# Kernel optimization log

Measured on AMD Instinct MI355X. Metric: run time of the kernel, lower is better.

The kernel has to match this reference:

```python
import jax, jax.numpy as jnp
import numpy as np

D_MODEL = 1024
NUM_HEAD = 16
D_HEAD = D_MODEL // NUM_HEAD


def setup_inputs() -> dict:
    key = jax.random.key(0)
    kx, kq, kk, kv, ko = jax.random.split(key, 5)
    x = jax.random.normal(kx, (2, 2048, D_MODEL), dtype=jnp.float32)
    p_q = jax.random.normal(kq, (D_MODEL, D_MODEL), dtype=jnp.float32)
    p_k = jax.random.normal(kk, (D_MODEL, D_MODEL), dtype=jnp.float32)
    p_v = jax.random.normal(kv, (D_MODEL, D_MODEL), dtype=jnp.float32)
    p_o = jax.random.normal(ko, (D_MODEL, D_MODEL), dtype=jnp.float32)
    return {"x": x, "p_q": p_q, "p_k": p_k, "p_v": p_v, "p_o": p_o}


def reference(x, p_q, p_k, p_v, p_o):
    B, S, _ = x.shape
    # project: weight viewed as [H, d_head, d_model]; out[b,h,s,d] = sum_m x[b,s,m] W[h,d,m]
    wq = p_q.reshape(NUM_HEAD, D_HEAD, D_MODEL)
    wk = p_k.reshape(NUM_HEAD, D_HEAD, D_MODEL)
    wv = p_v.reshape(NUM_HEAD, D_HEAD, D_MODEL)
    q = jnp.einsum('bsm,hdm->bhsd', x, wq)
    k = jnp.einsum('bsm,hdm->bhsd', x, wk)
    v = jnp.einsum('bsm,hdm->bhsd', x, wv)
    # full causal attention, scores scaled by 1/sqrt(d_head)
    scores = jnp.einsum('bhqd,bhkd->bhqk', q, k) / jnp.sqrt(jnp.float32(D_HEAD))
    causal = jnp.tril(jnp.ones((S, S), dtype=bool))
    scores = jnp.where(causal, scores, -jnp.inf)
    attn = jax.nn.softmax(scores, axis=-1)
    out = jnp.einsum('bhqk,bhkd->bhqd', attn, v)
    out = out.transpose(0, 2, 1, 3).reshape(B, S, D_MODEL)  # [B,S,H*d_head]
    # output proj: einsum '... d1, d2 d1 -> ... d2' == out @ p_o.T
    return jnp.einsum('bsm,nm->bsn', out, p_o)
```

## Files before the change

### kernel.cpp

```cpp
#include <hip/hip_runtime.h>
#include <stdint.h>

#define D_MODEL 1024
#define SEQ     2048
#define NHEAD   16
#define BATCH   2
#define NROWS   (BATCH*SEQ)

typedef _Float16 f16;
typedef _Float16 f16x8 __attribute__((ext_vector_type(8)));
typedef _Float16 f16x4 __attribute__((ext_vector_type(4)));
typedef __fp16   h16x2 __attribute__((ext_vector_type(2)));
typedef float    f32x4 __attribute__((ext_vector_type(4)));

#define MFMA16 __builtin_amdgcn_mfma_f32_16x16x32_f16

__device__ __forceinline__ void gload16(const void* g, void* l) {
  __builtin_amdgcn_global_load_lds(
      (const __attribute__((address_space(1))) void*)g,
      (__attribute__((address_space(3))) void*)l, 16, 0, 0);
}

__device__ __forceinline__ int pkh2(float a, float b) {
  union { h16x2 h; int i; } u;
  u.h = __builtin_amdgcn_cvt_pkrtz(a, b);
  return u.i;
}

__global__ void split4_kernel(const float* __restrict__ in, f16* __restrict__ hi,
                              f16* __restrict__ lo, int n4, float scale) {
  int i = blockIdx.x * blockDim.x + threadIdx.x;
  if (i >= n4) return;
  float4 v = reinterpret_cast<const float4*>(in)[i];
  v.x *= scale; v.y *= scale; v.z *= scale; v.w *= scale;
  f16x4 h, l4;
  h[0] = (f16)v.x; h[1] = (f16)v.y; h[2] = (f16)v.z; h[3] = (f16)v.w;
  l4[0] = (f16)(v.x - (float)h[0]);
  l4[1] = (f16)(v.y - (float)h[1]);
  l4[2] = (f16)(v.z - (float)h[2]);
  l4[3] = (f16)(v.w - (float)h[3]);
  *reinterpret_cast<f16x4*>(hi + 4*(size_t)i) = h;
  *reinterpret_cast<f16x4*>(lo + 4*(size_t)i) = l4;
}

__global__ void prep_w_kernel(const float* __restrict__ pq, const float* __restrict__ pk,
                              const float* __restrict__ pv, const float* __restrict__ po,
                              f16* __restrict__ wq_hi, f16* __restrict__ wq_lo,
                              f16* __restrict__ wk_hi, f16* __restrict__ wk_lo,
                              f16* __restrict__ wv_h,  f16* __restrict__ wo_h,
                              int n4, float qscale) {
  int i = blockIdx.x * blockDim.x + threadIdx.x;
  if (i >= n4) return;
  {
    float4 v = reinterpret_cast<const float4*>(pq)[i];
    v.x *= qscale; v.y *= qscale; v.z *= qscale; v.w *= qscale;
    f16x4 h, l4;
    h[0] = (f16)v.x; h[1] = (f16)v.y; h[2] = (f16)v.z; h[3] = (f16)v.w;
    l4[0] = (f16)(v.x - (float)h[0]); l4[1] = (f16)(v.y - (float)h[1]);
    l4[2] = (f16)(v.z - (float)h[2]); l4[3] = (f16)(v.w - (float)h[3]);
    *reinterpret_cast<f16x4*>(wq_hi + 4*(size_t)i) = h;
    *reinterpret_cast<f16x4*>(wq_lo + 4*(size_t)i) = l4;
  }
  {
    float4 v = reinterpret_cast<const float4*>(pk)[i];
    f16x4 h, l4;
    h[0] = (f16)v.x; h[1] = (f16)v.y; h[2] = (f16)v.z; h[3] = (f16)v.w;
    l4[0] = (f16)(v.x - (float)h[0]); l4[1] = (f16)(v.y - (float)h[1]);
    l4[2] = (f16)(v.z - (float)h[2]); l4[3] = (f16)(v.w - (float)h[3]);
    *reinterpret_cast<f16x4*>(wk_hi + 4*(size_t)i) = h;
    *reinterpret_cast<f16x4*>(wk_lo + 4*(size_t)i) = l4;
  }
  {
    float4 v = reinterpret_cast<const float4*>(pv)[i];
    f16x4 h;
    h[0] = (f16)v.x; h[1] = (f16)v.y; h[2] = (f16)v.z; h[3] = (f16)v.w;
    *reinterpret_cast<f16x4*>(wv_h + 4*(size_t)i) = h;
  }
  {
    float4 v = reinterpret_cast<const float4*>(po)[i];
    f16x4 h;
    h[0] = (f16)v.x; h[1] = (f16)v.y; h[2] = (f16)v.z; h[3] = (f16)v.w;
    *reinterpret_cast<f16x4*>(wo_h + 4*(size_t)i) = h;
  }
}

template<bool F32_OUT, bool COLCHUNK>
__global__ __launch_bounds__(256, 2)
void gemm_nt(const f16* __restrict__ Ahi,
             const f16* __restrict__ Bhi,
             f16* __restrict__ Chi, float* __restrict__ Cf,
             int M, int N, int K)
{
  constexpr int B_OFF  = 8192;
  constexpr int STRIDE = 12288;
  __shared__ __align__(16) char smem[2 * STRIDE];

  const int tid = threadIdx.x;
  const int w = tid >> 6, l = tid & 63;
  const int wr = (w >> 1) * 64;
  const int wc = (w & 1) * 32;

  const int gx = gridDim.x, gy = gridDim.y;
  const int nwg = gx * gy;
  const int flat = blockIdx.y * gx + blockIdx.x;
  const int swz = (flat & 7) * (nwg >> 3) + (flat >> 3);
  const int bxn = COLCHUNK ? (swz / gy) : (swz % gx);
  const int byn = COLCHUNK ? (swz % gy) : (swz / gx);
  const int bm = byn * 128, bn = bxn * 64;

  f32x4 acc[4][2] = {};

  const int srow = tid >> 2;
  const int schunk = 8 * (((tid & 3) ^ ((srow >> 1) & 3)));

  auto stage = [&](int kt) {
    char* dst = smem + (kt & 1) * STRIDE;
    const int k0 = kt * 32;
    const f16* ga = Ahi + (size_t)(bm + srow) * K + k0 + schunk;
    gload16(ga,        dst + (w << 10));
    gload16(ga + 64*K, dst + 4096 + (w << 10));
    const f16* gb = Bhi + (size_t)(bn + srow) * K + k0 + schunk;
    gload16(gb,        dst + B_OFF + (w << 10));
  };

  const int nkt = K >> 5;
  stage(0);

  for (int kt = 0; kt < nkt; kt++) {
    if (kt + 1 < nkt) {
      stage(kt + 1);
      asm volatile("s_waitcnt vmcnt(3)" ::: "memory");
    } else {
      asm volatile("s_waitcnt vmcnt(0)" ::: "memory");
    }
    __builtin_amdgcn_s_barrier();

    const char* buf = smem + (kt & 1) * STRIDE;
    const int ar = (l & 15);
    const int ak = 16 * ((l >> 4) ^ ((ar >> 1) & 3));
    f16x8 a_hi[4];
#pragma unroll
    for (int mi = 0; mi < 4; mi++)
      a_hi[mi] = *(const f16x8*)(buf + (size_t)(wr + mi*16 + ar) * 64 + ak);
    __builtin_amdgcn_s_setprio(1);
#pragma unroll
    for (int ni = 0; ni < 2; ni++) {
      f16x8 b_hi = *(const f16x8*)(buf + B_OFF + (size_t)(wc + ni*16 + ar) * 64 + ak);
#pragma unroll
      for (int mi = 0; mi < 4; mi++)
        acc[mi][ni] = MFMA16(a_hi[mi], b_hi, acc[mi][ni], 0, 0, 0);
    }
    __builtin_amdgcn_s_setprio(0);
    __builtin_amdgcn_s_barrier();
  }

  const int crow0 = bm + wr + (l >> 4) * 4;
  const int ccol0 = bn + wc + (l & 15);
#pragma unroll
  for (int mi = 0; mi < 4; mi++) {
#pragma unroll
    for (int ni = 0; ni < 2; ni++) {
#pragma unroll
      for (int j = 0; j < 4; j++) {
        size_t idx = (size_t)(crow0 + mi*16 + j) * N + (ccol0 + ni*16);
        float v = acc[mi][ni][j];
        if (F32_OUT) Cf[idx] = v;
        else         Chi[idx] = (f16)v;
      }
    }
  }
}

__global__ __launch_bounds__(256, 2)
void gemm_qkv(const f16* __restrict__ Ahi, const f16* __restrict__ Alo,
              const f16* __restrict__ Bqh, const f16* __restrict__ Bql,
              const f16* __restrict__ Bkh, const f16* __restrict__ Bkl,
              const f16* __restrict__ Bvh,
              f16* __restrict__ Qh, f16* __restrict__ Qlo2,
              f16* __restrict__ Kh, f16* __restrict__ Klo2,
              f16* __restrict__ VT)
{
  constexpr int N = D_MODEL, K = D_MODEL;
  constexpr int STRIDE = 36864;
  __shared__ __align__(16) char smem[2 * STRIDE];

  const int tid = threadIdx.x;
  const int w = tid >> 6, l = tid & 63;
  const int wr = (w >> 1) * 64;
  const int wc = (w & 1) * 32;

  const int flat = blockIdx.y * 16 + blockIdx.x;
  const int swz = (flat & 7) * 64 + (flat >> 3);
  const int bm = (swz / 16) * 128, bn = (swz % 16) * 64;

  f32x4 accQ[4][2] = {}, accK[4][2] = {}, accV[4][2] = {};

  const int srow = tid >> 2;
  const int schunk = 8 * (((tid & 3) ^ ((srow >> 1) & 3)));

  auto stage = [&](int kt) {
    char* dst = smem + (kt & 1) * STRIDE;
    const int k0 = kt * 32;
    const f16* ga = Ahi + (size_t)(bm + srow) * K + k0 + schunk;
    gload16(ga,        dst + (w << 10));
    gload16(ga + 64*K, dst + 4096 + (w << 10));
    const f16* gal = Alo + (size_t)(bm + srow) * K + k0 + schunk;
    gload16(gal,        dst + 8192 + (w << 10));
    gload16(gal + 64*K, dst + 12288 + (w << 10));
    const size_t bo = (size_t)(bn + srow) * K + k0 + schunk;
    gload16(Bqh + bo, dst + 16384 + (w << 10));
    gload16(Bql + bo, dst + 20480 + (w << 10));
    gload16(Bkh + bo, dst + 24576 + (w << 10));
    gload16(Bkl + bo, dst + 28672 + (w << 10));
    gload16(Bvh + bo, dst + 32768 + (w << 10));
  };

  const int nkt = K >> 5;
  stage(0);

  for (int kt = 0; kt < nkt; kt++) {
    if (kt + 1 < nkt) {
      stage(kt + 1);
      asm volatile("s_waitcnt vmcnt(9)" ::: "memory");
    } else {
      asm volatile("s_waitcnt vmcnt(0)" ::: "memory");
    }
    __builtin_amdgcn_s_barrier();

    const char* buf = smem + (kt & 1) * STRIDE;
    const int ar = (l & 15);
    const int ak = 16 * ((l >> 4) ^ ((ar >> 1) & 3));
    f16x8 a_hi[4], a_lo[4];
#pragma unroll
    for (int mi = 0; mi < 4; mi++) {
      a_hi[mi] = *(const f16x8*)(buf + (size_t)(wr + mi*16 + ar) * 64 + ak);
      a_lo[mi] = *(const f16x8*)(buf + 8192 + (size_t)(wr + mi*16 + ar) * 64 + ak);
    }
    __builtin_amdgcn_s_setprio(1);
#pragma unroll
    for (int ni = 0; ni < 2; ni++) {
      const int bo = (wc + ni*16 + ar) * 64 + ak;
      f16x8 bqh = *(const f16x8*)(buf + 16384 + bo);
      f16x8 bql = *(const f16x8*)(buf + 20480 + bo);
      f16x8 bkh = *(const f16x8*)(buf + 24576 + bo);
      f16x8 bkl = *(const f16x8*)(buf + 28672 + bo);
      f16x8 bvh = *(const f16x8*)(buf + 32768 + bo);
#pragma unroll
      for (int mi = 0; mi < 4; mi++) {
        accQ[mi][ni] = MFMA16(a_hi[mi], bqh, accQ[mi][ni], 0, 0, 0);
        accQ[mi][ni] = MFMA16(a_hi[mi], bql, accQ[mi][ni], 0, 0, 0);
        accQ[mi][ni] = MFMA16(a_lo[mi], bqh, accQ[mi][ni], 0, 0, 0);
        accK[mi][ni] = MFMA16(a_hi[mi], bkh, accK[mi][ni], 0, 0, 0);
        accK[mi][ni] = MFMA16(a_hi[mi], bkl, accK[mi][ni], 0, 0, 0);
        accK[mi][ni] = MFMA16(a_lo[mi], bkh, accK[mi][ni], 0, 0, 0);
        accV[mi][ni] = MFMA16(a_hi[mi], bvh, accV[mi][ni], 0, 0, 0);
      }
    }
    __builtin_amdgcn_s_setprio(0);
    __builtin_amdgcn_s_barrier();
  }

  const int crow0 = bm + wr + (l >> 4) * 4;
  const int ccol0 = bn + wc + (l & 15);
#pragma unroll
  for (int mi = 0; mi < 4; mi++) {
#pragma unroll
    for (int ni = 0; ni < 2; ni++) {
#pragma unroll
      for (int j = 0; j < 4; j++) {
        size_t idx = (size_t)(crow0 + mi*16 + j) * N + (ccol0 + ni*16);
        float qv = accQ[mi][ni][j];
        f16 qh = (f16)qv;
        Qh[idx] = qh;  Qlo2[idx] = (f16)(qv - (float)qh);
        float kv = accK[mi][ni][j];
        f16 kh = (f16)kv;
        Kh[idx] = kh;  Klo2[idx] = (f16)(kv - (float)kh);
      }
    }
  }

  {
    f16* tl = (f16*)smem;
#pragma unroll
    for (int mi = 0; mi < 4; mi++) {
#pragma unroll
      for (int ni = 0; ni < 2; ni++) {
        f16x4 v;
#pragma unroll
        for (int j = 0; j < 4; j++) v[j] = (f16)accV[mi][ni][j];
        const int m_l = wc + ni*16 + (l & 15);
        const int n_l = wr + mi*16 + ((l >> 4) << 2);
        *reinterpret_cast<f16x4*>(tl + m_l*136 + n_l) = v;
      }
    }
    __syncthreads();
    const int m_l = tid >> 2, cg = tid & 3;
    const size_t vbase = (size_t)(bn + m_l) * NROWS + bm + cg*32;
#pragma unroll
    for (int k2 = 0; k2 < 4; k2++) {
      f16x8 v = *reinterpret_cast<const f16x8*>(tl + m_l*136 + cg*32 + k2*8);
      *reinterpret_cast<f16x8*>(VT + vbase + k2*8) = v;
    }
  }
}

__global__ __launch_bounds__(512, 4)
void attn_kernel(const f16* __restrict__ Qhi, const f16* __restrict__ Qlo,
                 const f16* __restrict__ Khi, const f16* __restrict__ Klo,
                 const f16* __restrict__ VT, f16* __restrict__ Out)
{
  __shared__ __align__(16) char smem[49152];

  const int tid = threadIdx.x, w = tid >> 6, l = tid & 63;
  const int g = l >> 4, q4 = l & 15;
  const int wi = w & 3, grp = w >> 2;
  const int flat = blockIdx.x;
  const int xcd = flat & 7, slot = flat >> 3;
  const int bh = xcd * 4 + (slot >> 4);
  const int c = slot & 15;
  const int b = bh >> 4, h = bh & 15;
  const int bS = b * SEQ;
  const size_t hoff = (size_t)h * 64;
  const int T  = 64 - 2 * c;
  const int P1 = 2 * c + 2;
  const int P2 = 31 - 2 * c;

  int qw = (grp ? (31 - c) : c) * 64 + wi * 16;

  f16x8 qh[2], ql[2];
  auto loadQ = [&]() {
#pragma unroll
    for (int ks = 0; ks < 2; ks++) {
      const size_t base = (size_t)(bS + qw + q4) * D_MODEL + hoff + ks * 32 + g * 8;
      qh[ks] = *(const f16x8*)(Qhi + base);
      ql[ks] = *(const f16x8*)(Qlo + base);
    }
  };
  loadQ();

  f32x4 o[4] = {};
  float m_run = -INFINITY, l_run = 0.f;

  const int k_src = 8 * ((l & 7) ^ (l >> 3));
  const int v_src = 8 * ((l & 3) ^ ((l >> 2) & 3));
  const int rowloc = w * 8 + (l >> 3);

  const int idx_lo = (q4 + 32 * (g & 1)) * 4;
  const int idx_hi = idx_lo + 64;
  const bool upper = (l >= 32);

  auto stage64 = [&](int t) {
    const int kv0 = t * 64;
    char* dst = smem + (t & 1) * 24576;
    const size_t krow = (size_t)(bS + kv0 + rowloc) * D_MODEL + hoff + k_src;
    gload16(Khi + krow, dst + (w << 10));
    gload16(Klo + krow, dst + 8192 + (w << 10));
    const size_t vrow = (hoff + rowloc) * (size_t)NROWS + bS + kv0 + k_src;
    gload16(VT + vrow, dst + 16384 + (w << 10));
  };

  auto compute64 = [&](int t) {
    const char* buf = smem + (t & 1) * 24576;
    const int kv0 = t * 64;

    f32x4 s[4] = {};
    __builtin_amdgcn_s_setprio(1);
#pragma unroll
    for (int ni = 0; ni < 4; ni++) {
      const int row = ni * 16 + q4;
#pragma unroll
      for (int ks = 0; ks < 2; ks++) {
        const int boff = row * 128 + 16 * ((ks * 4 + g) ^ (row & 7));
        f16x8 kh8 = *(const f16x8*)(buf + boff);
        f16x8 kl8 = *(const f16x8*)(buf + 8192 + boff);
        s[ni] = MFMA16(kh8, qh[ks], s[ni], 0, 0, 0);
        s[ni] = MFMA16(kh8, ql[ks], s[ni], 0, 0, 0);
        s[ni] = MFMA16(kl8, qh[ks], s[ni], 0, 0, 0);
      }
    }
    __builtin_amdgcn_s_setprio(0);

    const bool need_mask = (kv0 + 63) > qw;
    const int q_abs = qw + q4;
    float p[4][4];
    float pm = -INFINITY;
#pragma unroll
    for (int ni = 0; ni < 4; ni++)
#pragma unroll
      for (int j = 0; j < 4; j++) {
        float v = s[ni][j];
        if (need_mask && (kv0 + ni * 16 + 4 * g + j) > q_abs) v = -INFINITY;
        p[ni][j] = v;
        pm = fmaxf(pm, v);
      }
    pm = fmaxf(pm, __shfl_xor(pm, 16));
    pm = fmaxf(pm, __shfl_xor(pm, 32));

    if (!__all(pm - m_run <= 8.0f)) {
      const float mn = fmaxf(m_run, pm);
      const float sc2 = __builtin_amdgcn_exp2f(m_run - mn);
      m_run = mn;
      l_run *= sc2;
#pragma unroll
      for (int nd = 0; nd < 4; nd++)
#pragma unroll
        for (int j = 0; j < 4; j++) o[nd][j] *= sc2;
    }
    float ps = 0.f;
#pragma unroll
    for (int ni = 0; ni < 4; ni++)
#pragma unroll
      for (int j = 0; j < 4; j++) {
        const float e = __builtin_amdgcn_exp2f(p[ni][j] - m_run);
        p[ni][j] = e;
        ps += e;
      }
    ps += __shfl_xor(ps, 16);
    ps += __shfl_xor(ps, 32);
    l_run += ps;

    f16x8 pa[2];
#pragma unroll
    for (int h2 = 0; h2 < 2; h2++) {
      const int pk0 = pkh2(p[2*h2][0],   p[2*h2][1]);
      const int pk1 = pkh2(p[2*h2][2],   p[2*h2][3]);
      const int pk2 = pkh2(p[2*h2+1][0], p[2*h2+1][1]);
      const int pk3 = pkh2(p[2*h2+1][2], p[2*h2+1][3]);
      const int b0l = __builtin_amdgcn_ds_bpermute(idx_lo, pk0);
      const int b2l = __builtin_amdgcn_ds_bpermute(idx_lo, pk2);
      const int b1l = __builtin_amdgcn_ds_bpermute(idx_lo, pk1);
      const int b3l = __builtin_amdgcn_ds_bpermute(idx_lo, pk3);
      const int b0h = __builtin_amdgcn_ds_bpermute(idx_hi, pk0);
      const int b2h = __builtin_amdgcn_ds_bpermute(idx_hi, pk2);
      const int b1h = __builtin_amdgcn_ds_bpermute(idx_hi, pk1);
      const int b3h = __builtin_amdgcn_ds_bpermute(idx_hi, pk3);
      union { int u[4]; f16x8 v; } pu;
      pu.u[0] = upper ? b2l : b0l;
      pu.u[1] = upper ? b3l : b1l;
      pu.u[2] = upper ? b2h : b0h;
      pu.u[3] = upper ? b3h : b1h;
      pa[h2] = pu.v;
    }

    __builtin_amdgcn_s_setprio(1);
#pragma unroll
    for (int nd = 0; nd < 4; nd++) {
      const int d = nd * 16 + q4;
#pragma unroll
      for (int h2 = 0; h2 < 2; h2++) {
        f16x8 bv = *(const f16x8*)(buf + 16384 + d * 128 + 16 * ((h2 * 4 + g) ^ (d & 7)));
        o[nd] = MFMA16(bv, pa[h2], o[nd], 0, 0, 0);
      }
    }
    __builtin_amdgcn_s_setprio(0);
  };

  auto stage32 = [&](int t) {
    const int kv0 = t * 32;
    char* sb = smem + (t & 3) * 12288;
    if (w < 4) {
      const f16* src = (w < 2) ? Khi : Klo;
      char* dstc = sb + ((w < 2) ? 0 : 4096);
      const int wi2 = w & 1;
#pragma unroll
      for (int gi = 0; gi < 2; gi++) {
        const int sub = 2 * wi2 + gi;
        const int row = 8 * sub + (l >> 3);
        gload16(src + (size_t)(bS + kv0 + row) * D_MODEL + hoff + k_src,
                dstc + sub * 1024);
      }
    } else if (w < 6) {
      const int wi2 = w - 4;
#pragma unroll
      for (int gi = 0; gi < 2; gi++) {
        const int sub = 2 * wi2 + gi;
        const int drow = 16 * sub + (l >> 2);
        gload16(VT + (hoff + drow) * (size_t)NROWS + bS + kv0 + v_src,
                sb + 8192 + sub * 1024);
      }
    }
  };

  auto compute32 = [&](int t) {
    const char* sb = smem + (t & 3) * 12288;
    const int kv0 = t * 32;

    f32x4 s[2] = {};
    __builtin_amdgcn_s_setprio(1);
#pragma unroll
    for (int ni = 0; ni < 2; ni++) {
      const int row = ni * 16 + q4;
#pragma unroll
      for (int ks = 0; ks < 2; ks++) {
        const int boff = row * 128 + 16 * ((ks * 4 + g) ^ (row & 7));
        f16x8 kh8 = *(const f16x8*)(sb + boff);
        f16x8 kl8 = *(const f16x8*)(sb + 4096 + boff);
        s[ni] = MFMA16(kh8, qh[ks], s[ni], 0, 0, 0);
        s[ni] = MFMA16(kh8, ql[ks], s[ni], 0, 0, 0);
        s[ni] = MFMA16(kl8, qh[ks], s[ni], 0, 0, 0);
      }
    }
    __builtin_amdgcn_s_setprio(0);

    const bool need_mask = (kv0 + 31) > qw;
    const int q_abs = qw + q4;
    float p[2][4];
    float pm = -INFINITY;
#pragma unroll
    for (int ni = 0; ni < 2; ni++)
#pragma unroll
      for (int j = 0; j < 4; j++) {
        float v = s[ni][j];
        if (need_mask && (kv0 + ni * 16 + 4 * g + j) > q_abs) v = -INFINITY;
        p[ni][j] = v;
        pm = fmaxf(pm, v);
      }
    pm = fmaxf(pm, __shfl_xor(pm, 16));
    pm = fmaxf(pm, __shfl_xor(pm, 32));

    if (!__all(pm - m_run <= 8.0f)) {
      const float mn = fmaxf(m_run, pm);
      const float sc2 = __builtin_amdgcn_exp2f(m_run - mn);
      m_run = mn;
      l_run *= sc2;
#pragma unroll
      for (int nd = 0; nd < 4; nd++)
#pragma unroll
        for (int j = 0; j < 4; j++) o[nd][j] *= sc2;
    }
    float ps = 0.f;
#pragma unroll
    for (int ni = 0; ni < 2; ni++)
#pragma unroll
      for (int j = 0; j < 4; j++) {
        const float e = __builtin_amdgcn_exp2f(p[ni][j] - m_run);
        p[ni][j] = e;
        ps += e;
      }
    ps += __shfl_xor(ps, 16);
    ps += __shfl_xor(ps, 32);
    l_run += ps;

    const int pk0 = pkh2(p[0][0], p[0][1]);
    const int pk1 = pkh2(p[0][2], p[0][3]);
    const int pk2 = pkh2(p[1][0], p[1][1]);
    const int pk3 = pkh2(p[1][2], p[1][3]);
    const int b0l = __builtin_amdgcn_ds_bpermute(idx_lo, pk0);
    const int b2l = __builtin_amdgcn_ds_bpermute(idx_lo, pk2);
    const int b1l = __builtin_amdgcn_ds_bpermute(idx_lo, pk1);
    const int b3l = __builtin_amdgcn_ds_bpermute(idx_lo, pk3);
    const int b0h = __builtin_amdgcn_ds_bpermute(idx_hi, pk0);
    const int b2h = __builtin_amdgcn_ds_bpermute(idx_hi, pk2);
    const int b1h = __builtin_amdgcn_ds_bpermute(idx_hi, pk1);
    const int b3h = __builtin_amdgcn_ds_bpermute(idx_hi, pk3);
    union { int u[4]; f16x8 v; } pu;
    pu.u[0] = upper ? b2l : b0l;
    pu.u[1] = upper ? b3l : b1l;
    pu.u[2] = upper ? b2h : b0h;
    pu.u[3] = upper ? b3h : b1h;
    const f16x8 pa = pu.v;

    __builtin_amdgcn_s_setprio(1);
#pragma unroll
    for (int nd = 0; nd < 4; nd++) {
      const int d = nd * 16 + q4;
      f16x8 bv = *(const f16x8*)(sb + 8192 + d * 64 + 16 * (g ^ (d & 3)));
      o[nd] = MFMA16(bv, pa, o[nd], 0, 0, 0);
    }
    __builtin_amdgcn_s_setprio(0);
  };

  stage64(0);
  for (int t = 0; t <= c; t++) {
    if (t + 1 <= c) {
      stage64(t + 1);
      asm volatile("s_waitcnt vmcnt(3)" ::: "memory");
    } else {
      asm volatile("s_waitcnt vmcnt(0)" ::: "memory");
    }
    __builtin_amdgcn_s_barrier();
    compute64(t);
    __builtin_amdgcn_s_barrier();
  }

  if (grp == 0) {
    const float inv = 1.0f / l_run;
    const size_t rowb = (size_t)(bS + qw + q4) * D_MODEL + hoff;
#pragma unroll
    for (int nd = 0; nd < 4; nd++) {
      f16x4 v;
#pragma unroll
      for (int j = 0; j < 4; j++) v[j] = (f16)(o[nd][j] * inv);
      *reinterpret_cast<f16x4*>(Out + rowb + nd * 16 + 4 * g) = v;
    }
    qw = (31 - c) * 64 + wi * 16;
    loadQ();
#pragma unroll
    for (int nd = 0; nd < 4; nd++)
#pragma unroll
      for (int j = 0; j < 4; j++) o[nd][j] = 0.f;
    m_run = -INFINITY;
    l_run = 0.f;
  }

  stage32(P1);
  stage32(P1 + 1);
  for (int j = 0; j < P2; j++) {
    const int u = P1 + 2 * j;
    const bool st = (u + 3) < T;
    if (st) { stage32(u + 2); stage32(u + 3); }
    if (st) asm volatile("s_waitcnt vmcnt(4)" ::: "memory");
    else    asm volatile("s_waitcnt vmcnt(0)" ::: "memory");
    __builtin_amdgcn_s_barrier();
    compute32(u + grp);
    __builtin_amdgcn_s_barrier();
  }

  if (grp == 0) {
    float* mb = (float*)smem + wi * 1152 + l * 18;
#pragma unroll
    for (int nd = 0; nd < 4; nd++)
#pragma unroll
      for (int j = 0; j < 4; j++) mb[nd * 4 + j] = o[nd][j];
    mb[16] = m_run;
    mb[17] = l_run;
  }
  __syncthreads();
  if (grp == 1) {
    const float* mb = (const float*)smem + wi * 1152 + l * 18;
    const float m2 = mb[16], l2 = mb[17];
    const float mm = fmaxf(m_run, m2);
    const float a1 = __builtin_amdgcn_exp2f(m_run - mm);
    const float a2 = __builtin_amdgcn_exp2f(m2 - mm);
    const float inv = 1.0f / (l_run * a1 + l2 * a2);
    const size_t rowb = (size_t)(bS + qw + q4) * D_MODEL + hoff;
#pragma unroll
    for (int nd = 0; nd < 4; nd++) {
      f16x4 v;
#pragma unroll
      for (int j = 0; j < 4; j++)
        v[j] = (f16)((o[nd][j] * a1 + mb[nd * 4 + j] * a2) * inv);
      *reinterpret_cast<f16x4*>(Out + rowb + nd * 16 + 4 * g) = v;
    }
  }
}

extern "C" void kernel_launch(void* const* d_in, const int* in_sizes, int n_in,
                              void* d_out, int out_size, void* d_ws, size_t ws_size,
                              hipStream_t stream) {
  const float* x  = (const float*)d_in[0];
  const float* pq = (const float*)d_in[1];
  const float* pk = (const float*)d_in[2];
  const float* pv = (const float*)d_in[3];
  const float* po = (const float*)d_in[4];
  float* out = (float*)d_out;

  char* ws = (char*)d_ws;
  size_t off = 0;
  auto alloc = [&](size_t elems) {
    f16* p = (f16*)(ws + off);
    off += ((elems * 2 + 255) & ~(size_t)255);
    return p;
  };
  f16* x_hi  = alloc((size_t)NROWS * D_MODEL);
  f16* x_lo  = alloc((size_t)NROWS * D_MODEL);
  f16* wq_hi = alloc((size_t)D_MODEL * D_MODEL);
  f16* wq_lo = alloc((size_t)D_MODEL * D_MODEL);
  f16* wk_hi = alloc((size_t)D_MODEL * D_MODEL);
  f16* wk_lo = alloc((size_t)D_MODEL * D_MODEL);
  f16* wv_h  = alloc((size_t)D_MODEL * D_MODEL);
  f16* wo_h  = alloc((size_t)D_MODEL * D_MODEL);
  f16* q_hi  = alloc((size_t)NROWS * D_MODEL);
  f16* q_lo  = alloc((size_t)NROWS * D_MODEL);
  f16* k_hi  = alloc((size_t)NROWS * D_MODEL);
  f16* k_lo  = alloc((size_t)NROWS * D_MODEL);
  f16* vt    = alloc((size_t)NROWS * D_MODEL);
  f16* ao    = alloc((size_t)NROWS * D_MODEL);

  const int n4x = NROWS * D_MODEL / 4;
  const int n4w = D_MODEL * D_MODEL / 4;
  const float qscale = 0.125f * 1.44269504088896f;
  split4_kernel<<<n4x/256, 256, 0, stream>>>(x, x_hi, x_lo, n4x, 1.0f);
  prep_w_kernel<<<n4w/256, 256, 0, stream>>>(pq, pk, pv, po,
                                             wq_hi, wq_lo, wk_hi, wk_lo, wv_h, wo_h,
                                             n4w, qscale);

  gemm_qkv<<<dim3(16, 32), 256, 0, stream>>>(x_hi, x_lo, wq_hi, wq_lo, wk_hi, wk_lo,
                                             wv_h, q_hi, q_lo, k_hi, k_lo, vt);

  attn_kernel<<<dim3(512), 512, 0, stream>>>(q_hi, q_lo, k_hi, k_lo, vt, ao);

  dim3 gg(D_MODEL/64, NROWS/128);
  gemm_nt<true, false><<<gg, 256, 0, stream>>>(ao, wo_h, nullptr, out, NROWS, D_MODEL, D_MODEL);
}
```

Measured before the change: 157.0 us.

## Replace 32-wide second-phase KV tiles with 64-wide triple-buffered tiles

```diff
diff --git a/kernel.cpp b/kernel.cpp
--- a/kernel.cpp
+++ b/kernel.cpp
@@ -309,7 +309,7 @@
                  const f16* __restrict__ Khi, const f16* __restrict__ Klo,
                  const f16* __restrict__ VT, f16* __restrict__ Out)
 {
-  __shared__ __align__(16) char smem[49152];
+  __shared__ __align__(16) char smem[73728];
 
   const int tid = threadIdx.x, w = tid >> 6, l = tid & 63;
   const int g = l >> 4, q4 = l & 15;
@@ -321,9 +321,7 @@
   const int b = bh >> 4, h = bh & 15;
   const int bS = b * SEQ;
   const size_t hoff = (size_t)h * 64;
-  const int T  = 64 - 2 * c;
-  const int P1 = 2 * c + 2;
-  const int P2 = 31 - 2 * c;
+  const int TB = 31 - c;
 
   int qw = (grp ? (31 - c) : c) * 64 + wi * 16;
 
@@ -342,16 +340,15 @@
   float m_run = -INFINITY, l_run = 0.f;
 
   const int k_src = 8 * ((l & 7) ^ (l >> 3));
-  const int v_src = 8 * ((l & 3) ^ ((l >> 2) & 3));
   const int rowloc = w * 8 + (l >> 3);
 
   const int idx_lo = (q4 + 32 * (g & 1)) * 4;
   const int idx_hi = idx_lo + 64;
   const bool upper = (l >= 32);
 
-  auto stage64 = [&](int t) {
+  auto stage64 = [&](int t, int slot3) {
     const int kv0 = t * 64;
-    char* dst = smem + (t & 1) * 24576;
+    char* dst = smem + slot3 * 24576;
     const size_t krow = (size_t)(bS + kv0 + rowloc) * D_MODEL + hoff + k_src;
     gload16(Khi + krow, dst + (w << 10));
     gload16(Klo + krow, dst + 8192 + (w << 10));
@@ -359,8 +356,8 @@
     gload16(VT + vrow, dst + 16384 + (w << 10));
   };
 
-  auto compute64 = [&](int t) {
-    const char* buf = smem + (t & 1) * 24576;
+  auto compute64 = [&](int t, int slot3) {
+    const char* buf = smem + slot3 * 24576;
     const int kv0 = t * 64;
 
     f32x4 s[4] = {};
@@ -455,131 +452,16 @@
     __builtin_amdgcn_s_setprio(0);
   };
 
-  auto stage32 = [&](int t) {
-    const int kv0 = t * 32;
-    char* sb = smem + (t & 3) * 12288;
-    if (w < 4) {
-      const f16* src = (w < 2) ? Khi : Klo;
-      char* dstc = sb + ((w < 2) ? 0 : 4096);
-      const int wi2 = w & 1;
-#pragma unroll
-      for (int gi = 0; gi < 2; gi++) {
-        const int sub = 2 * wi2 + gi;
-        const int row = 8 * sub + (l >> 3);
-        gload16(src + (size_t)(bS + kv0 + row) * D_MODEL + hoff + k_src,
-                dstc + sub * 1024);
-      }
-    } else if (w < 6) {
-      const int wi2 = w - 4;
-#pragma unroll
-      for (int gi = 0; gi < 2; gi++) {
-        const int sub = 2 * wi2 + gi;
-        const int drow = 16 * sub + (l >> 2);
-        gload16(VT + (hoff + drow) * (size_t)NROWS + bS + kv0 + v_src,
-                sb + 8192 + sub * 1024);
-      }
-    }
-  };
-
-  auto compute32 = [&](int t) {
-    const char* sb = smem + (t & 3) * 12288;
-    const int kv0 = t * 32;
-
-    f32x4 s[2] = {};
-    __builtin_amdgcn_s_setprio(1);
-#pragma unroll
-    for (int ni = 0; ni < 2; ni++) {
-      const int row = ni * 16 + q4;
-#pragma unroll
-      for (int ks = 0; ks < 2; ks++) {
-        const int boff = row * 128 + 16 * ((ks * 4 + g) ^ (row & 7));
-        f16x8 kh8 = *(const f16x8*)(sb + boff);
-        f16x8 kl8 = *(const f16x8*)(sb + 4096 + boff);
-        s[ni] = MFMA16(kh8, qh[ks], s[ni], 0, 0, 0);
-        s[ni] = MFMA16(kh8, ql[ks], s[ni], 0, 0, 0);
-        s[ni] = MFMA16(kl8, qh[ks], s[ni], 0, 0, 0);
-      }
-    }
-    __builtin_amdgcn_s_setprio(0);
-
-    const bool need_mask = (kv0 + 31) > qw;
-    const int q_abs = qw + q4;
-    float p[2][4];
-    float pm = -INFINITY;
-#pragma unroll
-    for (int ni = 0; ni < 2; ni++)
-#pragma unroll
-      for (int j = 0; j < 4; j++) {
-        float v = s[ni][j];
-        if (need_mask && (kv0 + ni * 16 + 4 * g + j) > q_abs) v = -INFINITY;
-        p[ni][j] = v;
-        pm = fmaxf(pm, v);
-      }
-    pm = fmaxf(pm, __shfl_xor(pm, 16));
-    pm = fmaxf(pm, __shfl_xor(pm, 32));
-
-    if (!__all(pm - m_run <= 8.0f)) {
-      const float mn = fmaxf(m_run, pm);
-      const float sc2 = __builtin_amdgcn_exp2f(m_run - mn);
-      m_run = mn;
-      l_run *= sc2;
-#pragma unroll
-      for (int nd = 0; nd < 4; nd++)
-#pragma unroll
-        for (int j = 0; j < 4; j++) o[nd][j] *= sc2;
-    }
-    float ps = 0.f;
-#pragma unroll
-    for (int ni = 0; ni < 2; ni++)
-#pragma unroll
-      for (int j = 0; j < 4; j++) {
-        const float e = __builtin_amdgcn_exp2f(p[ni][j] - m_run);
-        p[ni][j] = e;
-        ps += e;
-      }
-    ps += __shfl_xor(ps, 16);
-    ps += __shfl_xor(ps, 32);
-    l_run += ps;
-
-    const int pk0 = pkh2(p[0][0], p[0][1]);
-    const int pk1 = pkh2(p[0][2], p[0][3]);
-    const int pk2 = pkh2(p[1][0], p[1][1]);
-    const int pk3 = pkh2(p[1][2], p[1][3]);
-    const int b0l = __builtin_amdgcn_ds_bpermute(idx_lo, pk0);
-    const int b2l = __builtin_amdgcn_ds_bpermute(idx_lo, pk2);
-    const int b1l = __builtin_amdgcn_ds_bpermute(idx_lo, pk1);
-    const int b3l = __builtin_amdgcn_ds_bpermute(idx_lo, pk3);
-    const int b0h = __builtin_amdgcn_ds_bpermute(idx_hi, pk0);
-    const int b2h = __builtin_amdgcn_ds_bpermute(idx_hi, pk2);
-    const int b1h = __builtin_amdgcn_ds_bpermute(idx_hi, pk1);
-    const int b3h = __builtin_amdgcn_ds_bpermute(idx_hi, pk3);
-    union { int u[4]; f16x8 v; } pu;
-    pu.u[0] = upper ? b2l : b0l;
-    pu.u[1] = upper ? b3l : b1l;
-    pu.u[2] = upper ? b2h : b0h;
-    pu.u[3] = upper ? b3h : b1h;
-    const f16x8 pa = pu.v;
-
-    __builtin_amdgcn_s_setprio(1);
-#pragma unroll
-    for (int nd = 0; nd < 4; nd++) {
-      const int d = nd * 16 + q4;
-      f16x8 bv = *(const f16x8*)(sb + 8192 + d * 64 + 16 * (g ^ (d & 3)));
-      o[nd] = MFMA16(bv, pa, o[nd], 0, 0, 0);
-    }
-    __builtin_amdgcn_s_setprio(0);
-  };
-
-  stage64(0);
+  stage64(0, 0);
   for (int t = 0; t <= c; t++) {
     if (t + 1 <= c) {
-      stage64(t + 1);
+      stage64(t + 1, (t + 1) & 1);
       asm volatile("s_waitcnt vmcnt(3)" ::: "memory");
     } else {
       asm volatile("s_waitcnt vmcnt(0)" ::: "memory");
     }
     __builtin_amdgcn_s_barrier();
-    compute64(t);
+    compute64(t, t & 1);
     __builtin_amdgcn_s_barrier();
   }
 
@@ -603,19 +485,29 @@
     l_run = 0.f;
   }
 
-  stage32(P1);
-  stage32(P1 + 1);
-  for (int j = 0; j < P2; j++) {
-    const int u = P1 + 2 * j;
-    const bool st = (u + 3) < T;
-    if (st) { stage32(u + 2); stage32(u + 3); }
-    if (st) asm volatile("s_waitcnt vmcnt(4)" ::: "memory");
-    else    asm volatile("s_waitcnt vmcnt(0)" ::: "memory");
-    __builtin_amdgcn_s_barrier();
-    compute32(u + grp);
-    __builtin_amdgcn_s_barrier();
-  }
-
+  {
+    const int u0 = c + 1;
+    stage64(u0, u0 % 3);
+    if (u0 + 1 <= TB) stage64(u0 + 1, (u0 + 1) % 3);
+    const int iters = (TB - u0) / 2 + 1;
+    for (int j = 0; j < iters; j++) {
+      const int u = u0 + 2 * j;
+      const bool pf1 = (u + 2) <= TB;
+      if (pf1) {
+        stage64(u + 2, (u + 2) % 3);
+        asm volatile("s_waitcnt vmcnt(3)" ::: "memory");
+      } else {
+        asm volatile("s_waitcnt vmcnt(0)" ::: "memory");
+      }
+      __builtin_amdgcn_s_barrier();
+      if (grp == 0)          compute64(u, u % 3);
+      else if (u + 1 <= TB)  compute64(u + 1, (u + 1) % 3);
+      __builtin_amdgcn_s_barrier();
+      if ((u + 3) <= TB) stage64(u + 3, (u + 3) % 3);
+    }
+  }
+
+  __builtin_amdgcn_s_barrier();
   if (grp == 0) {
     float* mb = (float*)smem + wi * 1152 + l * 18;
 #pragma unroll
```

Result: faster. 150.9 us (-3.9%).
